# Optimization experiments

Measured on AMD Instinct MI355X. Metric: run time of the kernel, lower is better.

## Reference

```python
import jax, jax.numpy as jnp
import numpy as np

B, S, D, H = 2, 2048, 512, 8
HD = D // H
EPS = 1e-8
SCALE = HD ** -0.5


def setup_inputs() -> dict:
    key = jax.random.key(0)
    ks = jax.random.split(key, 12)
    gene_emb = jax.random.normal(ks[0], (B, S, D), jnp.float32)
    expr_emb = jax.random.normal(ks[1], (B, S, D), jnp.float32)
    M = jax.random.randint(ks[2], (B, S, S), 0, 2).astype(jnp.float32)
    def lin(k, fan_in, fan_out):
        kw, kb = jax.random.split(k)
        bound = 1.0 / np.sqrt(fan_in)
        W = jax.random.uniform(kw, (fan_in, fan_out), jnp.float32, -bound, bound)
        b = jax.random.uniform(kb, (fan_out,), jnp.float32, -bound, bound)
        return W, b
    Wf, bf = lin(ks[3], 2 * D, D)  # fused_emb_proj
    Wq, bq = lin(ks[4], D, D)
    Wk, bk = lin(ks[5], D, D)
    Wv, bv = lin(ks[6], D, D)
    Wo, bo = lin(ks[7], D, D)
    return {"gene_emb": gene_emb, "expr_emb": expr_emb, "M": M,
            "Wf": Wf, "bf": bf, "Wq": Wq, "bq": bq, "Wk": Wk, "bk": bk,
            "Wv": Wv, "bv": bv, "Wo": Wo, "bo": bo}


def reference(gene_emb, expr_emb, M, Wf, bf, Wq, bq, Wk, bk, Wv, bv, Wo, bo):
    # fused=True, self_attention=False path: Q and K from projected concat
    fused = jnp.concatenate([gene_emb, expr_emb], axis=-1) @ Wf + bf  # [B,S,D]
    Q = (fused @ Wq + bq).reshape(B, S, H, HD)
    K = (fused @ Wk + bk).reshape(B, S, H, HD)
    V = (expr_emb @ Wv + bv).reshape(B, S, H, HD)
    scores = jnp.einsum('bqhd,bkhd->bhqk', Q, K) * SCALE  # [B,H,S,S]
    Mh = M[:, None, :, :]  # broadcast over heads
    scores = scores + jnp.where(Mh == 0, -1e9, 0.0)
    attn = jax.nn.softmax(scores, axis=-1)
    A = attn * Mh  # gated weights
    A = A / (jnp.sum(jnp.abs(A), axis=-1, keepdims=True) + EPS)  # abs-sum renorm
    out = jnp.einsum('bhqk,bkhd->bqhd', A, V).reshape(B, S, D)
    return out @ Wo + bo
```

## Files before the change

kernel.cpp:

```cpp
#include <hip/hip_runtime.h>
#include <stdint.h>
#include <math.h>

#define BB 2
#define SS 2048
#define DDIM 512
#define HH 8
#define HDD 64
static constexpr float SCALE = 0.125f;

typedef unsigned short u16;
typedef short bf16x8 __attribute__((ext_vector_type(8)));
typedef float f32x4 __attribute__((ext_vector_type(4)));

__device__ __forceinline__ u16 f2bf(float x) {
  unsigned int u = __float_as_uint(x);
  unsigned int r = (u + 0x7fffu + ((u >> 16) & 1u)) >> 16;
  return (u16)r;
}

__device__ __forceinline__ void cp16(const void* g, void* l) {
  __builtin_amdgcn_global_load_lds(
      (const __attribute__((address_space(1))) void*)g,
      (__attribute__((address_space(3))) void*)l, 16, 0, 0);
}

__global__ __launch_bounds__(256) void cast_bf16_k(
    const float* __restrict__ g, const float* __restrict__ e,
    u16* __restrict__ og, u16* __restrict__ oe) {
  int i = blockIdx.x * 256 + threadIdx.x;
  float4 a = ((const float4*)g)[i];
  float4 b = ((const float4*)e)[i];
  ushort4 ua, ub;
  ua.x = f2bf(a.x); ua.y = f2bf(a.y); ua.z = f2bf(a.z); ua.w = f2bf(a.w);
  ub.x = f2bf(b.x); ub.y = f2bf(b.y); ub.z = f2bf(b.z); ub.w = f2bf(b.w);
  ((ushort4*)og)[i] = ua;
  ((ushort4*)oe)[i] = ub;
}

__global__ __launch_bounds__(256) void wprep_k(
    const float* __restrict__ Wf, const float* __restrict__ Wq,
    const float* __restrict__ Wk, const float* __restrict__ Wv,
    const float* __restrict__ Wo,
    u16* __restrict__ WfT, u16* __restrict__ WqT, u16* __restrict__ WkT,
    u16* __restrict__ WvT, u16* __restrict__ WoT) {
  int z = blockIdx.z;
  const float* W; u16* WT; int K;
  switch (z) {
    case 0: W = Wf; WT = WfT; K = 1024; break;
    case 1: W = Wq; WT = WqT; K = 512; break;
    case 2: W = Wk; WT = WkT; K = 512; break;
    case 3: W = Wv; WT = WvT; K = 512; break;
    default: W = Wo; WT = WoT; K = 512; break;
  }
  int k0 = blockIdx.y * 32;
  if (k0 >= K) return;
  int n0 = blockIdx.x * 32;
  __shared__ float t[32][33];
  int tx = threadIdx.x & 31, ty = threadIdx.x >> 5;
#pragma unroll
  for (int i = 0; i < 32; i += 8)
    t[ty + i][tx] = W[(size_t)(k0 + ty + i) * DDIM + n0 + tx];
  __syncthreads();
#pragma unroll
  for (int i = 0; i < 32; i += 8)
    WT[(size_t)(n0 + ty + i) * K + k0 + tx] = f2bf(t[tx][ty + i]);
}

template <int EPI>
__global__ __launch_bounds__(256) void gemm_k(
    const u16* __restrict__ A0, const u16* __restrict__ A1,
    const u16* __restrict__ Bt0, const u16* __restrict__ Bt1,
    const u16* __restrict__ Bt2,
    const float* __restrict__ bias0, const float* __restrict__ bias1,
    const float* __restrict__ bias2,
    u16* __restrict__ O0, u16* __restrict__ O1, u16* __restrict__ O2,
    float* __restrict__ OF) {
  constexpr int BK = 32;
  __shared__ alignas(16) u16 Al[64 * BK];
  __shared__ alignas(16) u16 Bl[64 * BK];

  const int tid = threadIdx.x;
  const int l = tid & 63, w = tid >> 6, lg = l >> 4, lr = l & 15;
  const int wm = w >> 1, wn = w & 1;
  const int m0 = blockIdx.y * 64;
  const int n0 = blockIdx.x * 64;
  const int Ksz = (EPI == 0) ? 1024 : 512;

  const u16* Aa = A0; const u16* Bt = Bt0; const float* bias = bias0;
  int z = 0;
  if (EPI == 1) {
    z = blockIdx.z;
    Aa = (z == 2) ? A1 : A0;
    Bt = (z == 0) ? Bt0 : (z == 1) ? Bt1 : Bt2;
    bias = (z == 0) ? bias0 : (z == 1) ? bias1 : bias2;
  }

  f32x4 zero4 = {0.f, 0.f, 0.f, 0.f};
  f32x4 acc[2][2];
#pragma unroll
  for (int i = 0; i < 2; ++i)
#pragma unroll
    for (int j = 0; j < 2; ++j) acc[i][j] = zero4;

  const int arow = tid >> 2;
  const int apos = tid & 3;
  const int k8s = apos ^ ((arow >> 1) & 3);

  for (int k0 = 0; k0 < Ksz; k0 += BK) {
    __syncthreads();
    {
      int kg = k0 + 8 * k8s;
      const u16* src;
      if (EPI == 0) {
        src = (kg < 512) ? (A0 + (size_t)(m0 + arow) * 512 + kg)
                         : (A1 + (size_t)(m0 + arow) * 512 + (kg - 512));
      } else {
        src = Aa + (size_t)(m0 + arow) * 512 + kg;
      }
      cp16(src, (char*)Al + (size_t)arow * 64 + apos * 16);
    }
    {
      const u16* src = Bt + (size_t)(n0 + arow) * Ksz + k0 + 8 * k8s;
      cp16(src, (char*)Bl + (size_t)arow * 64 + apos * 16);
    }
    asm volatile("s_waitcnt vmcnt(0)" ::: "memory");
    __syncthreads();

    bf16x8 af[2], bfr[2];
#pragma unroll
    for (int i = 0; i < 2; ++i) {
      int row = 32 * wm + 16 * i + lr;
      af[i] = *(const bf16x8*)((const char*)Al + row * 64 +
                               ((lg ^ ((row >> 1) & 3)) * 16));
    }
#pragma unroll
    for (int j = 0; j < 2; ++j) {
      int row = 32 * wn + 16 * j + lr;
      bfr[j] = *(const bf16x8*)((const char*)Bl + row * 64 +
                                ((lg ^ ((row >> 1) & 3)) * 16));
    }
#pragma unroll
    for (int i = 0; i < 2; ++i)
#pragma unroll
      for (int j = 0; j < 2; ++j)
        acc[i][j] =
            __builtin_amdgcn_mfma_f32_16x16x32_bf16(af[i], bfr[j], acc[i][j], 0, 0, 0);
  }

#pragma unroll
  for (int j = 0; j < 2; ++j) {
    int c = n0 + 32 * wn + 16 * j + lr;
    float bv = bias[c];
#pragma unroll
    for (int i = 0; i < 2; ++i) {
      int qb = m0 + 32 * wm + 16 * i + 4 * lg;
      if (EPI == 0) {
#pragma unroll
        for (int r = 0; r < 4; ++r)
          O0[(size_t)(qb + r) * 512 + c] = f2bf(acc[i][j][r] + bv);
      } else if (EPI == 2) {
#pragma unroll
        for (int r = 0; r < 4; ++r)
          OF[(size_t)(qb + r) * 512 + c] = acc[i][j][r] + bv;
      } else {
        int b = qb >> 11, s = qb & 2047;
        int hh = c >> 6, hd = c & 63;
        if (z < 2) {
          u16* O = (z == 0) ? O0 : O1;
#pragma unroll
          for (int r = 0; r < 4; ++r)
            O[((size_t)(b * HH + hh) * SS + s + r) * HDD + hd] =
                f2bf(acc[i][j][r] + bv);
        } else {
          ushort4 v;
          v.x = f2bf(acc[i][j][0] + bv);
          v.y = f2bf(acc[i][j][1] + bv);
          v.z = f2bf(acc[i][j][2] + bv);
          v.w = f2bf(acc[i][j][3] + bv);
          *(ushort4*)(O2 + ((size_t)(b * HH + hh) * HDD + hd) * SS + s) = v;
        }
      }
    }
  }
}

__global__ __launch_bounds__(512) void attn2_k(
    const u16* __restrict__ Qh, const u16* __restrict__ Kh,
    const u16* __restrict__ Vt, const float* __restrict__ Mm,
    u16* __restrict__ AO) {
  __shared__ alignas(16) u16 Kl[2][64 * 64];
  __shared__ alignas(16) u16 Vl[2][64 * 64];
  __shared__ alignas(16) u16 Pl[8][16 * 64];

  const int tid = threadIdx.x;
  const int l = tid & 63, w = tid >> 6, lg = l >> 4, lr = l & 15;
  const int qg = w & 3, kh = w >> 2;
  const int bh = blockIdx.y, b = bh >> 3, h = bh & 7;
  const int qw = blockIdx.x * 64 + 16 * qg;

  bf16x8 qf[2];
  {
    const u16* qp = Qh + ((size_t)bh * SS + qw + lr) * HDD + 8 * lg;
    qf[0] = *(const bf16x8*)qp;
    qf[1] = *(const bf16x8*)(qp + 32);
  }
  f32x4 zero4 = {0.f, 0.f, 0.f, 0.f};
  f32x4 o[4];
#pragma unroll
  for (int t = 0; t < 4; ++t) o[t] = zero4;
  float mrun[4] = {-INFINITY, -INFINITY, -INFINITY, -INFINITY};
  float lrun[4] = {0.f, 0.f, 0.f, 0.f};

  const float* Mb = Mm + ((size_t)b * SS + qw + 4 * lg) * SS;

  const int srow = tid >> 3;
  const int spos = tid & 7;
  const int sk8 = spos ^ (srow & 7);
  const size_t sdst = (size_t)tid * 16;

  for (int kt = 0; kt < 16; ++kt) {
    const int kb0 = kt * 64, kb1 = 1024 + kt * 64;
    __syncthreads();
    cp16(Kh + ((size_t)bh * SS + kb0 + srow) * HDD + 8 * sk8, (char*)Kl[0] + sdst);
    cp16(Vt + ((size_t)bh * HDD + srow) * SS + kb0 + 8 * sk8, (char*)Vl[0] + sdst);
    cp16(Kh + ((size_t)bh * SS + kb1 + srow) * HDD + 8 * sk8, (char*)Kl[1] + sdst);
    cp16(Vt + ((size_t)bh * HDD + srow) * SS + kb1 + 8 * sk8, (char*)Vl[1] + sdst);
    asm volatile("s_waitcnt vmcnt(0)" ::: "memory");
    __syncthreads();

    const int kb = kh * 1024 + kt * 64;
    const u16* Klw = Kl[kh];
    const u16* Vlw = Vl[kh];

    f32x4 sc[4];
#pragma unroll
    for (int ct = 0; ct < 4; ++ct) {
      int krow = 16 * ct + lr;
      const char* kbase = (const char*)Klw + krow * 128;
      bf16x8 k0f = *(const bf16x8*)(kbase + ((lg) ^ (krow & 7)) * 16);
      bf16x8 k1f = *(const bf16x8*)(kbase + ((4 + lg) ^ (krow & 7)) * 16);
      f32x4 zz = zero4;
      zz = __builtin_amdgcn_mfma_f32_16x16x32_bf16(qf[0], k0f, zz, 0, 0, 0);
      zz = __builtin_amdgcn_mfma_f32_16x16x32_bf16(qf[1], k1f, zz, 0, 0, 0);
      sc[ct] = zz;
    }
#pragma unroll
    for (int ct = 0; ct < 4; ++ct) {
#pragma unroll
      for (int r = 0; r < 4; ++r) {
        float mv = Mb[(size_t)r * SS + kb + 16 * ct + lr];
        sc[ct][r] = (mv != 0.0f) ? sc[ct][r] * SCALE : -INFINITY;
      }
    }
#pragma unroll
    for (int r = 0; r < 4; ++r) {
      float t = fmaxf(fmaxf(sc[0][r], sc[1][r]), fmaxf(sc[2][r], sc[3][r]));
      t = fmaxf(t, __shfl_xor(t, 1));
      t = fmaxf(t, __shfl_xor(t, 2));
      t = fmaxf(t, __shfl_xor(t, 4));
      t = fmaxf(t, __shfl_xor(t, 8));
      float mnew = fmaxf(mrun[r], t);
      float fac = (mnew == -INFINITY) ? 1.0f : __expf(mrun[r] - mnew);
      float psum = 0.f;
#pragma unroll
      for (int ct = 0; ct < 4; ++ct) {
        float p = (sc[ct][r] == -INFINITY) ? 0.f : __expf(sc[ct][r] - mnew);
        sc[ct][r] = p;
        psum += p;
      }
      psum += __shfl_xor(psum, 1);
      psum += __shfl_xor(psum, 2);
      psum += __shfl_xor(psum, 4);
      psum += __shfl_xor(psum, 8);
      mrun[r] = mnew;
      lrun[r] = lrun[r] * fac + psum;
#pragma unroll
      for (int t4 = 0; t4 < 4; ++t4) o[t4][r] *= fac;
    }
    u16* Pw = Pl[w];
#pragma unroll
    for (int ct = 0; ct < 4; ++ct) {
#pragma unroll
      for (int r = 0; r < 4; ++r) {
        int row = 4 * lg + r;
        int col = 16 * ct + lr;
        int pos = (col >> 3) ^ (row & 7);
        Pw[row * 64 + pos * 8 + (col & 7)] = f2bf(sc[ct][r]);
      }
    }
#pragma unroll
    for (int kk = 0; kk < 2; ++kk) {
      bf16x8 pf = *(const bf16x8*)((const char*)Pw + lr * 128 +
                                   (((4 * kk + lg) ^ (lr & 7)) * 16));
#pragma unroll
      for (int t4 = 0; t4 < 4; ++t4) {
        int vrow = 16 * t4 + lr;
        bf16x8 vf = *(const bf16x8*)((const char*)Vlw + vrow * 128 +
                                     (((4 * kk + lg) ^ (vrow & 7)) * 16));
        o[t4] = __builtin_amdgcn_mfma_f32_16x16x32_bf16(pf, vf, o[t4], 0, 0, 0);
      }
    }
  }

  __syncthreads();
  float* sh = (float*)Kl;
  if (kh == 1) {
    float* p = sh + ((size_t)(w - 4) * 64 + l) * 24;
#pragma unroll
    for (int r = 0; r < 4; ++r) { p[r] = mrun[r]; p[4 + r] = lrun[r]; }
#pragma unroll
    for (int t4 = 0; t4 < 4; ++t4)
#pragma unroll
      for (int r = 0; r < 4; ++r) p[8 + 4 * t4 + r] = o[t4][r];
  }
  __syncthreads();
  if (kh == 0) {
    const float* p = sh + ((size_t)w * 64 + l) * 24;
#pragma unroll
    for (int r = 0; r < 4; ++r) {
      float mB = p[r], lB = p[4 + r];
      float ms = fmaxf(mrun[r], mB);
      float fa = (mrun[r] > -INFINITY) ? __expf(mrun[r] - ms) : 0.f;
      float fb = (mB > -INFINITY) ? __expf(mB - ms) : 0.f;
      float ls = lrun[r] * fa + lB * fb;
      float inv = (ls > 0.f) ? 1.0f / (ls + 1e-8f) : 0.f;
      size_t row = (size_t)b * SS + qw + 4 * lg + r;
#pragma unroll
      for (int t4 = 0; t4 < 4; ++t4) {
        float ov = o[t4][r] * fa + p[8 + 4 * t4 + r] * fb;
        AO[row * DDIM + h * HDD + 16 * t4 + lr] = f2bf(ov * inv);
      }
    }
  }
}

extern "C" void kernel_launch(void* const* d_in, const int* in_sizes, int n_in,
                              void* d_out, int out_size, void* d_ws, size_t ws_size,
                              hipStream_t stream) {
  if (ws_size < (size_t)(31.5 * 1024 * 1024)) return;

  const float* gene = (const float*)d_in[0];
  const float* expr = (const float*)d_in[1];
  const float* Mm = (const float*)d_in[2];
  const float* Wf = (const float*)d_in[3];
  const float* bf = (const float*)d_in[4];
  const float* Wq = (const float*)d_in[5];
  const float* bq = (const float*)d_in[6];
  const float* Wk = (const float*)d_in[7];
  const float* bk = (const float*)d_in[8];
  const float* Wv = (const float*)d_in[9];
  const float* bv = (const float*)d_in[10];
  const float* Wo = (const float*)d_in[11];
  const float* bo = (const float*)d_in[12];
  float* out = (float*)d_out;

  char* ws = (char*)d_ws;
  const size_t MB4 = 4194304;
  u16* geneB = (u16*)(ws + 0 * MB4);
  u16* exprB = (u16*)(ws + 1 * MB4);
  u16* fusedB = (u16*)(ws + 2 * MB4);
  u16* QhB = (u16*)(ws + 3 * MB4);
  u16* KhB = (u16*)(ws + 4 * MB4);
  u16* VtB = (u16*)(ws + 5 * MB4);
  u16* attnB = (u16*)(ws + 6 * MB4);
  u16* WfT = (u16*)(ws + 7 * MB4);
  u16* WqT = (u16*)(ws + 7 * MB4 + 1048576);
  u16* WkT = (u16*)(ws + 7 * MB4 + 1048576 + 524288);
  u16* WvT = (u16*)(ws + 7 * MB4 + 1048576 + 2 * 524288);
  u16* WoT = (u16*)(ws + 7 * MB4 + 1048576 + 3 * 524288);

  cast_bf16_k<<<2048, 256, 0, stream>>>(gene, expr, geneB, exprB);
  wprep_k<<<dim3(16, 32, 5), 256, 0, stream>>>(Wf, Wq, Wk, Wv, Wo, WfT, WqT,
                                               WkT, WvT, WoT);
  gemm_k<0><<<dim3(8, 64), 256, 0, stream>>>(geneB, exprB, WfT, nullptr, nullptr,
                                             bf, nullptr, nullptr, fusedB,
                                             nullptr, nullptr, nullptr);
  gemm_k<1><<<dim3(8, 64, 3), 256, 0, stream>>>(fusedB, exprB, WqT, WkT, WvT,
                                                bq, bk, bv, QhB, KhB, VtB,
                                                nullptr);
  attn2_k<<<dim3(32, 16), 512, 0, stream>>>(QhB, KhB, VtB, Mm, attnB);
  gemm_k<2><<<dim3(8, 64), 256, 0, stream>>>(attnB, nullptr, WoT, nullptr,
                                             nullptr, bo, nullptr, nullptr,
                                             nullptr, nullptr, nullptr, out);
}
```

Baseline: 225.2 us.

## Pack mask into bitwords and double-buffer K/V in single-pass attention

Adds a pre-pass that packs the float mask into 64-bit ballot words, so the attention kernel reads 1 bit per key instead of 4 bytes. Each attention block now has 4 waves covering the full key range with double-buffered async K/V loads that prefetch the next tile during compute. This removes the split-key merge through LDS. The cost is an extra kernel launch, half as many threads per block, and a longer serial loop per wave. The packed mask reuses the workspace slot of geneB, which is safe only because the first GEMM has already consumed it.

```diff
diff --git a/kernel.cpp b/kernel.cpp
--- a/kernel.cpp
+++ b/kernel.cpp
@@ -10,6 +10,7 @@
 static constexpr float SCALE = 0.125f;
 
 typedef unsigned short u16;
+typedef unsigned long long u64;
 typedef short bf16x8 __attribute__((ext_vector_type(8)));
 typedef float f32x4 __attribute__((ext_vector_type(4)));
 
@@ -67,6 +68,21 @@
     WT[(size_t)(n0 + ty + i) * K + k0 + tx] = f2bf(t[tx][ty + i]);
 }
 
+__global__ __launch_bounds__(256) void mpack_k(const float* __restrict__ M,
+                                               u64* __restrict__ Mb) {
+  int wid = (blockIdx.x * 256 + threadIdx.x) >> 6;
+  int lane = threadIdx.x & 63;
+#pragma unroll 4
+  for (int i = 0; i < 64; ++i) {
+    size_t word = (size_t)wid * 64 + i;
+    size_t row = word >> 5;
+    int c0 = (int)(word & 31) * 64;
+    float mv = M[row * SS + c0 + lane];
+    u64 bits = __ballot(mv != 0.0f);
+    if (lane == 0) Mb[word] = bits;
+  }
+}
+
 template <int EPI>
 __global__ __launch_bounds__(256) void gemm_k(
     const u16* __restrict__ A0, const u16* __restrict__ A1,
@@ -185,19 +201,18 @@
   }
 }
 
-__global__ __launch_bounds__(512) void attn2_k(
+__global__ __launch_bounds__(256) void attn3_k(
     const u16* __restrict__ Qh, const u16* __restrict__ Kh,
-    const u16* __restrict__ Vt, const float* __restrict__ Mm,
+    const u16* __restrict__ Vt, const u64* __restrict__ Mbits,
     u16* __restrict__ AO) {
   __shared__ alignas(16) u16 Kl[2][64 * 64];
   __shared__ alignas(16) u16 Vl[2][64 * 64];
-  __shared__ alignas(16) u16 Pl[8][16 * 64];
+  __shared__ alignas(16) u16 Pl[4][16 * 64];
 
   const int tid = threadIdx.x;
   const int l = tid & 63, w = tid >> 6, lg = l >> 4, lr = l & 15;
-  const int qg = w & 3, kh = w >> 2;
   const int bh = blockIdx.y, b = bh >> 3, h = bh & 7;
-  const int qw = blockIdx.x * 64 + 16 * qg;
+  const int qw = blockIdx.x * 64 + 16 * w;
 
   bf16x8 qf[2];
   {
@@ -212,26 +227,48 @@
   float mrun[4] = {-INFINITY, -INFINITY, -INFINITY, -INFINITY};
   float lrun[4] = {0.f, 0.f, 0.f, 0.f};
 
-  const float* Mb = Mm + ((size_t)b * SS + qw + 4 * lg) * SS;
+  const u64* Mw = Mbits + ((size_t)b * SS + qw + 4 * lg) * 32;
 
   const int srow = tid >> 3;
   const int spos = tid & 7;
-  const int sk8 = spos ^ (srow & 7);
   const size_t sdst = (size_t)tid * 16;
 
-  for (int kt = 0; kt < 16; ++kt) {
-    const int kb0 = kt * 64, kb1 = 1024 + kt * 64;
-    __syncthreads();
-    cp16(Kh + ((size_t)bh * SS + kb0 + srow) * HDD + 8 * sk8, (char*)Kl[0] + sdst);
-    cp16(Vt + ((size_t)bh * HDD + srow) * SS + kb0 + 8 * sk8, (char*)Vl[0] + sdst);
-    cp16(Kh + ((size_t)bh * SS + kb1 + srow) * HDD + 8 * sk8, (char*)Kl[1] + sdst);
-    cp16(Vt + ((size_t)bh * HDD + srow) * SS + kb1 + 8 * sk8, (char*)Vl[1] + sdst);
-    asm volatile("s_waitcnt vmcnt(0)" ::: "memory");
-    __syncthreads();
-
-    const int kb = kh * 1024 + kt * 64;
-    const u16* Klw = Kl[kh];
-    const u16* Vlw = Vl[kh];
+#pragma unroll
+  for (int c = 0; c < 2; ++c) {
+    int row = srow + 32 * c;
+    int k8 = spos ^ (row & 7);
+    cp16(Kh + ((size_t)bh * SS + row) * HDD + 8 * k8, (char*)Kl[0] + sdst + c * 4096);
+    cp16(Vt + ((size_t)bh * HDD + row) * SS + 8 * k8, (char*)Vl[0] + sdst + c * 4096);
+  }
+  u64 mw[4];
+#pragma unroll
+  for (int r = 0; r < 4; ++r) mw[r] = Mw[r << 5];
+  asm volatile("s_waitcnt vmcnt(0)" ::: "memory");
+  __syncthreads();
+
+  int cur = 0;
+  for (int kt = 0; kt < 32; ++kt) {
+    if (kt < 31) {
+      const int kb1 = (kt + 1) * 64;
+#pragma unroll
+      for (int c = 0; c < 2; ++c) {
+        int row = srow + 32 * c;
+        int k8 = spos ^ (row & 7);
+        cp16(Kh + ((size_t)bh * SS + kb1 + row) * HDD + 8 * k8,
+             (char*)Kl[cur ^ 1] + sdst + c * 4096);
+        cp16(Vt + ((size_t)bh * HDD + row) * SS + kb1 + 8 * k8,
+             (char*)Vl[cur ^ 1] + sdst + c * 4096);
+      }
+    }
+    u64 mwN[4];
+    {
+      int ktn = (kt < 31) ? kt + 1 : kt;
+#pragma unroll
+      for (int r = 0; r < 4; ++r) mwN[r] = Mw[(r << 5) + ktn];
+    }
+
+    const u16* Klw = Kl[cur];
+    const u16* Vlw = Vl[cur];
 
     f32x4 sc[4];
 #pragma unroll
@@ -249,8 +286,8 @@
     for (int ct = 0; ct < 4; ++ct) {
 #pragma unroll
       for (int r = 0; r < 4; ++r) {
-        float mv = Mb[(size_t)r * SS + kb + 16 * ct + lr];
-        sc[ct][r] = (mv != 0.0f) ? sc[ct][r] * SCALE : -INFINITY;
+        bool keep = (mw[r] >> (16 * ct + lr)) & 1ull;
+        sc[ct][r] = keep ? sc[ct][r] * SCALE : -INFINITY;
       }
     }
 #pragma unroll
@@ -301,36 +338,21 @@
         o[t4] = __builtin_amdgcn_mfma_f32_16x16x32_bf16(pf, vf, o[t4], 0, 0, 0);
       }
     }
-  }
-
-  __syncthreads();
-  float* sh = (float*)Kl;
-  if (kh == 1) {
-    float* p = sh + ((size_t)(w - 4) * 64 + l) * 24;
-#pragma unroll
-    for (int r = 0; r < 4; ++r) { p[r] = mrun[r]; p[4 + r] = lrun[r]; }
-#pragma unroll
-    for (int t4 = 0; t4 < 4; ++t4)
-#pragma unroll
-      for (int r = 0; r < 4; ++r) p[8 + 4 * t4 + r] = o[t4][r];
-  }
-  __syncthreads();
-  if (kh == 0) {
-    const float* p = sh + ((size_t)w * 64 + l) * 24;
-#pragma unroll
-    for (int r = 0; r < 4; ++r) {
-      float mB = p[r], lB = p[4 + r];
-      float ms = fmaxf(mrun[r], mB);
-      float fa = (mrun[r] > -INFINITY) ? __expf(mrun[r] - ms) : 0.f;
-      float fb = (mB > -INFINITY) ? __expf(mB - ms) : 0.f;
-      float ls = lrun[r] * fa + lB * fb;
-      float inv = (ls > 0.f) ? 1.0f / (ls + 1e-8f) : 0.f;
-      size_t row = (size_t)b * SS + qw + 4 * lg + r;
-#pragma unroll
-      for (int t4 = 0; t4 < 4; ++t4) {
-        float ov = o[t4][r] * fa + p[8 + 4 * t4 + r] * fb;
-        AO[row * DDIM + h * HDD + 16 * t4 + lr] = f2bf(ov * inv);
-      }
+#pragma unroll
+    for (int r = 0; r < 4; ++r) mw[r] = mwN[r];
+    asm volatile("s_waitcnt vmcnt(0)" ::: "memory");
+    __syncthreads();
+    cur ^= 1;
+  }
+
+#pragma unroll
+  for (int r = 0; r < 4; ++r) {
+    float inv = (lrun[r] > 0.f) ? 1.0f / (lrun[r] + 1e-8f) : 0.f;
+    size_t row = (size_t)b * SS + qw + 4 * lg + r;
+#pragma unroll
+    for (int t4 = 0; t4 < 4; ++t4) {
+      int d = 16 * t4 + lr;
+      AO[row * DDIM + h * HDD + d] = f2bf(o[t4][r] * inv);
     }
   }
 }
@@ -369,6 +391,7 @@
   u16* WkT = (u16*)(ws + 7 * MB4 + 1048576 + 524288);
   u16* WvT = (u16*)(ws + 7 * MB4 + 1048576 + 2 * 524288);
   u16* WoT = (u16*)(ws + 7 * MB4 + 1048576 + 3 * 524288);
+  u64* MbB = (u64*)(ws + 0 * MB4);
 
   cast_bf16_k<<<2048, 256, 0, stream>>>(gene, expr, geneB, exprB);
   wprep_k<<<dim3(16, 32, 5), 256, 0, stream>>>(Wf, Wq, Wk, Wv, Wo, WfT, WqT,
@@ -376,10 +399,11 @@
   gemm_k<0><<<dim3(8, 64), 256, 0, stream>>>(geneB, exprB, WfT, nullptr, nullptr,
                                              bf, nullptr, nullptr, fusedB,
                                              nullptr, nullptr, nullptr);
+  mpack_k<<<512, 256, 0, stream>>>(Mm, MbB);
   gemm_k<1><<<dim3(8, 64, 3), 256, 0, stream>>>(fusedB, exprB, WqT, WkT, WvT,
                                                 bq, bk, bv, QhB, KhB, VtB,
                                                 nullptr);
-  attn2_k<<<dim3(32, 16), 512, 0, stream>>>(QhB, KhB, VtB, Mm, attnB);
+  attn3_k<<<dim3(32, 16), 256, 0, stream>>>(QhB, KhB, VtB, MbB, attnB);
   gemm_k<2><<<dim3(8, 64), 256, 0, stream>>>(attnB, nullptr, WoT, nullptr,
                                              nullptr, bo, nullptr, nullptr,
                                              nullptr, nullptr, nullptr, out);
```

Result: slower. 257.7 us (+14.4%).

## Bit-pack mask and restructure attention to load K/V directly into registers

Applied to the files above, without the earlier changes.

Adds a kernel that packs the float mask into 64-bit ballot bitmasks, so attention reads 1 bit per mask element instead of a 4-byte float. The attention kernel is rewritten to 256 threads with one KV pass per wave: it computes S^T (K as the A operand) so each lane holds a single query row's running max and sum, and it loads K/V fragments straight from global memory instead of staging them through LDS with block barriers. The split-KV merge is removed. The costs are redundant global/L2 reads of K/V across waves and an extra launch for packing the mask. The packed mask reuses workspace slot 0 (geneB), which is no longer needed by then.

```diff
diff --git a/kernel.cpp b/kernel.cpp
--- a/kernel.cpp
+++ b/kernel.cpp
@@ -10,6 +10,7 @@
 static constexpr float SCALE = 0.125f;
 
 typedef unsigned short u16;
+typedef unsigned long long u64;
 typedef short bf16x8 __attribute__((ext_vector_type(8)));
 typedef float f32x4 __attribute__((ext_vector_type(4)));
 
@@ -67,6 +68,26 @@
     WT[(size_t)(n0 + ty + i) * K + k0 + tx] = f2bf(t[tx][ty + i]);
 }
 
+__global__ __launch_bounds__(256) void mpack2_k(const float* __restrict__ M,
+                                                u64* __restrict__ Mp) {
+  int wid = (blockIdx.x * 256 + threadIdx.x) >> 6;
+  int lane = threadIdx.x & 63;
+#pragma unroll 4
+  for (int i = 0; i < 16; ++i) {
+    int idx = wid * 16 + i;
+    int row = idx >> 3, k = idx & 7;
+    float4 v = *(const float4*)&M[(size_t)row * SS + k * 256 + lane * 4];
+    u64 b0 = __ballot(v.x != 0.0f);
+    u64 b1 = __ballot(v.y != 0.0f);
+    u64 b2 = __ballot(v.z != 0.0f);
+    u64 b3 = __ballot(v.w != 0.0f);
+    if (lane == 0) {
+      u64* p = Mp + ((size_t)row * 32 + k * 4);
+      p[0] = b0; p[1] = b1; p[2] = b2; p[3] = b3;
+    }
+  }
+}
+
 template <int EPI>
 __global__ __launch_bounds__(256) void gemm_k(
     const u16* __restrict__ A0, const u16* __restrict__ A1,
@@ -185,153 +206,137 @@
   }
 }
 
-__global__ __launch_bounds__(512) void attn2_k(
+__global__ __launch_bounds__(256) void attn4_k(
     const u16* __restrict__ Qh, const u16* __restrict__ Kh,
-    const u16* __restrict__ Vt, const float* __restrict__ Mm,
+    const u16* __restrict__ Vt, const u64* __restrict__ Mp,
     u16* __restrict__ AO) {
-  __shared__ alignas(16) u16 Kl[2][64 * 64];
-  __shared__ alignas(16) u16 Vl[2][64 * 64];
-  __shared__ alignas(16) u16 Pl[8][16 * 64];
+  __shared__ alignas(16) u16 Pl[4][16 * 64];
 
   const int tid = threadIdx.x;
   const int l = tid & 63, w = tid >> 6, lg = l >> 4, lr = l & 15;
-  const int qg = w & 3, kh = w >> 2;
   const int bh = blockIdx.y, b = bh >> 3, h = bh & 7;
-  const int qw = blockIdx.x * 64 + 16 * qg;
-
-  bf16x8 qf[2];
+  const int qw = blockIdx.x * 64 + 16 * w;
+
+  const u16* Kb = Kh + (size_t)bh * SS * HDD;
+  const u16* Vb = Vt + (size_t)bh * HDD * SS;
+
+  bf16x8 qf0, qf1;
   {
     const u16* qp = Qh + ((size_t)bh * SS + qw + lr) * HDD + 8 * lg;
-    qf[0] = *(const bf16x8*)qp;
-    qf[1] = *(const bf16x8*)(qp + 32);
-  }
+    qf0 = *(const bf16x8*)qp;
+    qf1 = *(const bf16x8*)(qp + 32);
+  }
+
   f32x4 zero4 = {0.f, 0.f, 0.f, 0.f};
   f32x4 o[4];
 #pragma unroll
   for (int t = 0; t < 4; ++t) o[t] = zero4;
-  float mrun[4] = {-INFINITY, -INFINITY, -INFINITY, -INFINITY};
-  float lrun[4] = {0.f, 0.f, 0.f, 0.f};
-
-  const float* Mb = Mm + ((size_t)b * SS + qw + 4 * lg) * SS;
-
-  const int srow = tid >> 3;
-  const int spos = tid & 7;
-  const int sk8 = spos ^ (srow & 7);
-  const size_t sdst = (size_t)tid * 16;
-
-  for (int kt = 0; kt < 16; ++kt) {
-    const int kb0 = kt * 64, kb1 = 1024 + kt * 64;
-    __syncthreads();
-    cp16(Kh + ((size_t)bh * SS + kb0 + srow) * HDD + 8 * sk8, (char*)Kl[0] + sdst);
-    cp16(Vt + ((size_t)bh * HDD + srow) * SS + kb0 + 8 * sk8, (char*)Vl[0] + sdst);
-    cp16(Kh + ((size_t)bh * SS + kb1 + srow) * HDD + 8 * sk8, (char*)Kl[1] + sdst);
-    cp16(Vt + ((size_t)bh * HDD + srow) * SS + kb1 + 8 * sk8, (char*)Vl[1] + sdst);
-    asm volatile("s_waitcnt vmcnt(0)" ::: "memory");
-    __syncthreads();
-
-    const int kb = kh * 1024 + kt * 64;
-    const u16* Klw = Kl[kh];
-    const u16* Vlw = Vl[kh];
-
+  float mrun = -INFINITY, lrun = 0.f;
+
+  const u64* Mrow = Mp + ((size_t)b * SS + qw + lr) * 32;
+  u64 mp[4], mpN[4];
+#pragma unroll
+  for (int r = 0; r < 4; ++r) mp[r] = Mrow[r];
+
+  u16* Pw = Pl[w];
+
+  for (int kt = 0; kt < 32; ++kt) {
+    const int tm = kt & 3;
+    if (tm == 0 && kt < 28) {
+#pragma unroll
+      for (int r = 0; r < 4; ++r) mpN[r] = Mrow[((kt >> 2) + 1) * 4 + r];
+    }
+    bf16x8 kf[4][2];
+#pragma unroll
+    for (int g = 0; g < 4; ++g) {
+      const u16* kp = Kb + (size_t)(64 * kt + 16 * g + lr) * 64 + 8 * lg;
+      kf[g][0] = *(const bf16x8*)kp;
+      kf[g][1] = *(const bf16x8*)(kp + 32);
+    }
+    bf16x8 vf[4][2];
+#pragma unroll
+    for (int t4 = 0; t4 < 4; ++t4) {
+      const u16* vp = Vb + (size_t)(16 * t4 + lr) * SS + 64 * kt + 8 * lg;
+      vf[t4][0] = *(const bf16x8*)vp;
+      vf[t4][1] = *(const bf16x8*)(vp + 32);
+    }
     f32x4 sc[4];
 #pragma unroll
-    for (int ct = 0; ct < 4; ++ct) {
-      int krow = 16 * ct + lr;
-      const char* kbase = (const char*)Klw + krow * 128;
-      bf16x8 k0f = *(const bf16x8*)(kbase + ((lg) ^ (krow & 7)) * 16);
-      bf16x8 k1f = *(const bf16x8*)(kbase + ((4 + lg) ^ (krow & 7)) * 16);
+    for (int g = 0; g < 4; ++g) {
       f32x4 zz = zero4;
-      zz = __builtin_amdgcn_mfma_f32_16x16x32_bf16(qf[0], k0f, zz, 0, 0, 0);
-      zz = __builtin_amdgcn_mfma_f32_16x16x32_bf16(qf[1], k1f, zz, 0, 0, 0);
-      sc[ct] = zz;
-    }
-#pragma unroll
-    for (int ct = 0; ct < 4; ++ct) {
+      zz = __builtin_amdgcn_mfma_f32_16x16x32_bf16(kf[g][0], qf0, zz, 0, 0, 0);
+      zz = __builtin_amdgcn_mfma_f32_16x16x32_bf16(kf[g][1], qf1, zz, 0, 0, 0);
+      sc[g] = zz;
+    }
+#pragma unroll
+    for (int g = 0; g < 4; ++g)
 #pragma unroll
       for (int r = 0; r < 4; ++r) {
-        float mv = Mb[(size_t)r * SS + kb + 16 * ct + lr];
-        sc[ct][r] = (mv != 0.0f) ? sc[ct][r] * SCALE : -INFINITY;
+        bool keep = (mp[r] >> (16 * tm + 4 * g + lg)) & 1ull;
+        sc[g][r] = keep ? sc[g][r] * SCALE : -INFINITY;
       }
-    }
-#pragma unroll
-    for (int r = 0; r < 4; ++r) {
-      float t = fmaxf(fmaxf(sc[0][r], sc[1][r]), fmaxf(sc[2][r], sc[3][r]));
-      t = fmaxf(t, __shfl_xor(t, 1));
-      t = fmaxf(t, __shfl_xor(t, 2));
-      t = fmaxf(t, __shfl_xor(t, 4));
-      t = fmaxf(t, __shfl_xor(t, 8));
-      float mnew = fmaxf(mrun[r], t);
-      float fac = (mnew == -INFINITY) ? 1.0f : __expf(mrun[r] - mnew);
-      float psum = 0.f;
-#pragma unroll
-      for (int ct = 0; ct < 4; ++ct) {
-        float p = (sc[ct][r] == -INFINITY) ? 0.f : __expf(sc[ct][r] - mnew);
-        sc[ct][r] = p;
+    float t = -INFINITY;
+#pragma unroll
+    for (int g = 0; g < 4; ++g)
+#pragma unroll
+      for (int r = 0; r < 4; ++r) t = fmaxf(t, sc[g][r]);
+    t = fmaxf(t, __shfl_xor(t, 16));
+    t = fmaxf(t, __shfl_xor(t, 32));
+    float mnew = fmaxf(mrun, t);
+    float fac = (mnew == -INFINITY) ? 1.0f : __expf(mrun - mnew);
+    float psum = 0.f;
+#pragma unroll
+    for (int g = 0; g < 4; ++g)
+#pragma unroll
+      for (int r = 0; r < 4; ++r) {
+        float p = (sc[g][r] == -INFINITY) ? 0.f : __expf(sc[g][r] - mnew);
+        sc[g][r] = p;
         psum += p;
       }
-      psum += __shfl_xor(psum, 1);
-      psum += __shfl_xor(psum, 2);
-      psum += __shfl_xor(psum, 4);
-      psum += __shfl_xor(psum, 8);
-      mrun[r] = mnew;
-      lrun[r] = lrun[r] * fac + psum;
-#pragma unroll
-      for (int t4 = 0; t4 < 4; ++t4) o[t4][r] *= fac;
-    }
-    u16* Pw = Pl[w];
-#pragma unroll
-    for (int ct = 0; ct < 4; ++ct) {
-#pragma unroll
-      for (int r = 0; r < 4; ++r) {
-        int row = 4 * lg + r;
-        int col = 16 * ct + lr;
-        int pos = (col >> 3) ^ (row & 7);
-        Pw[row * 64 + pos * 8 + (col & 7)] = f2bf(sc[ct][r]);
-      }
+    psum += __shfl_xor(psum, 16);
+    psum += __shfl_xor(psum, 32);
+    mrun = mnew;
+    lrun = lrun * fac + psum;
+    float facr[4];
+#pragma unroll
+    for (int r = 0; r < 4; ++r) facr[r] = __shfl(fac, 4 * lg + r);
+#pragma unroll
+    for (int t4 = 0; t4 < 4; ++t4)
+#pragma unroll
+      for (int r = 0; r < 4; ++r) o[t4][r] *= facr[r];
+#pragma unroll
+    for (int g = 0; g < 4; ++g) {
+      unsigned int lo = (unsigned int)f2bf(sc[g][0]) |
+                        ((unsigned int)f2bf(sc[g][1]) << 16);
+      unsigned int hi = (unsigned int)f2bf(sc[g][2]) |
+                        ((unsigned int)f2bf(sc[g][3]) << 16);
+      uint2 pv = {lo, hi};
+      int c = 2 * g + (lg >> 1);
+      int byte = lr * 128 + ((c ^ (lr & 7)) * 16) + (lg & 1) * 8;
+      *(uint2*)((char*)Pw + byte) = pv;
     }
 #pragma unroll
     for (int kk = 0; kk < 2; ++kk) {
       bf16x8 pf = *(const bf16x8*)((const char*)Pw + lr * 128 +
                                    (((4 * kk + lg) ^ (lr & 7)) * 16));
 #pragma unroll
-      for (int t4 = 0; t4 < 4; ++t4) {
-        int vrow = 16 * t4 + lr;
-        bf16x8 vf = *(const bf16x8*)((const char*)Vlw + vrow * 128 +
-                                     (((4 * kk + lg) ^ (vrow & 7)) * 16));
-        o[t4] = __builtin_amdgcn_mfma_f32_16x16x32_bf16(pf, vf, o[t4], 0, 0, 0);
-      }
-    }
-  }
-
-  __syncthreads();
-  float* sh = (float*)Kl;
-  if (kh == 1) {
-    float* p = sh + ((size_t)(w - 4) * 64 + l) * 24;
-#pragma unroll
-    for (int r = 0; r < 4; ++r) { p[r] = mrun[r]; p[4 + r] = lrun[r]; }
+      for (int t4 = 0; t4 < 4; ++t4)
+        o[t4] = __builtin_amdgcn_mfma_f32_16x16x32_bf16(pf, vf[t4][kk], o[t4], 0, 0, 0);
+    }
+    if (tm == 3) {
+#pragma unroll
+      for (int r = 0; r < 4; ++r) mp[r] = mpN[r];
+    }
+  }
+
+  float inv = (lrun > 0.f) ? 1.0f / (lrun + 1e-8f) : 0.f;
+#pragma unroll
+  for (int r = 0; r < 4; ++r) {
+    float invr = __shfl(inv, 4 * lg + r);
+    size_t row = (size_t)b * SS + qw + 4 * lg + r;
 #pragma unroll
     for (int t4 = 0; t4 < 4; ++t4)
-#pragma unroll
-      for (int r = 0; r < 4; ++r) p[8 + 4 * t4 + r] = o[t4][r];
-  }
-  __syncthreads();
-  if (kh == 0) {
-    const float* p = sh + ((size_t)w * 64 + l) * 24;
-#pragma unroll
-    for (int r = 0; r < 4; ++r) {
-      float mB = p[r], lB = p[4 + r];
-      float ms = fmaxf(mrun[r], mB);
-      float fa = (mrun[r] > -INFINITY) ? __expf(mrun[r] - ms) : 0.f;
-      float fb = (mB > -INFINITY) ? __expf(mB - ms) : 0.f;
-      float ls = lrun[r] * fa + lB * fb;
-      float inv = (ls > 0.f) ? 1.0f / (ls + 1e-8f) : 0.f;
-      size_t row = (size_t)b * SS + qw + 4 * lg + r;
-#pragma unroll
-      for (int t4 = 0; t4 < 4; ++t4) {
-        float ov = o[t4][r] * fa + p[8 + 4 * t4 + r] * fb;
-        AO[row * DDIM + h * HDD + 16 * t4 + lr] = f2bf(ov * inv);
-      }
-    }
+      AO[row * DDIM + h * HDD + 16 * t4 + lr] = f2bf(o[t4][r] * invr);
   }
 }
 
@@ -369,6 +374,7 @@
   u16* WkT = (u16*)(ws + 7 * MB4 + 1048576 + 524288);
   u16* WvT = (u16*)(ws + 7 * MB4 + 1048576 + 2 * 524288);
   u16* WoT = (u16*)(ws + 7 * MB4 + 1048576 + 3 * 524288);
+  u64* MpB = (u64*)(ws + 0 * MB4);
 
   cast_bf16_k<<<2048, 256, 0, stream>>>(gene, expr, geneB, exprB);
   wprep_k<<<dim3(16, 32, 5), 256, 0, stream>>>(Wf, Wq, Wk, Wv, Wo, WfT, WqT,
@@ -376,10 +382,11 @@
   gemm_k<0><<<dim3(8, 64), 256, 0, stream>>>(geneB, exprB, WfT, nullptr, nullptr,
                                              bf, nullptr, nullptr, fusedB,
                                              nullptr, nullptr, nullptr);
+  mpack2_k<<<512, 256, 0, stream>>>(Mm, MpB);
   gemm_k<1><<<dim3(8, 64, 3), 256, 0, stream>>>(fusedB, exprB, WqT, WkT, WvT,
                                                 bq, bk, bv, QhB, KhB, VtB,
                                                 nullptr);
-  attn2_k<<<dim3(32, 16), 512, 0, stream>>>(QhB, KhB, VtB, Mm, attnB);
+  attn4_k<<<dim3(32, 16), 256, 0, stream>>>(QhB, KhB, VtB, MpB, attnB);
   gemm_k<2><<<dim3(8, 64), 256, 0, stream>>>(attnB, nullptr, WoT, nullptr,
                                              nullptr, bo, nullptr, nullptr,
                                              nullptr, nullptr, nullptr, out);
```

Measured after the change: 303.9 us. 1.35x slower.
